# Optimization experiments

Hardware: AMD Instinct MI355X
Metric: run time of the kernel (lower is better)

Reference implementation:

```python
import jax, jax.numpy as jnp
import numpy as np

N_NODES = 100000
N_EDGES = 3200000


def gcn_conv(x, src, dst, ew, W, b, num_nodes):
    """PyG GCNConv: h = x@W; out[dst] += norm * h[src]; norm = d^-1/2[src]*w*d^-1/2[dst].
    src/dst/ew must already include self-loops (weight 1)."""
    h = x @ W  # [N, F_out]
    deg = jax.ops.segment_sum(ew, dst, num_segments=num_nodes)  # weighted in-degree
    dinv = jnp.where(deg > 0, jax.lax.rsqrt(deg), 0.0)
    norm = dinv[src] * ew * dinv[dst]  # [E]
    msg = h[src] * norm[:, None]  # [E, F_out] gather + scale
    out = jax.ops.segment_sum(msg, dst, num_segments=num_nodes)  # scatter-add
    return out + b


def setup_inputs() -> dict:
    key = jax.random.key(0)
    k1, k2, k3, k4, k5 = jax.random.split(key, 5)
    x = jax.random.normal(k1, (N_NODES, 35), dtype=jnp.float32)
    edge_index = jax.random.randint(k2, (2, N_EDGES), 0, N_NODES, dtype=jnp.int64)
    edge_weight = jax.random.uniform(k3, (N_EDGES,), dtype=jnp.float32)
    W1 = jax.random.normal(k4, (35, 64), dtype=jnp.float32) * (1.0 / np.sqrt(35))
    b1 = jnp.zeros((64,), dtype=jnp.float32)
    W2 = jax.random.normal(k5, (64, 2), dtype=jnp.float32) * (1.0 / np.sqrt(64))
    b2 = jnp.zeros((2,), dtype=jnp.float32)
    return {"x": x, "edge_index": edge_index, "edge_weight": edge_weight,
            "W1": W1, "b1": b1, "W2": W2, "b2": b2}


def reference(x, edge_index, edge_weight, W1, b1, W2, b2):
    n = x.shape[0]
    # add self-loops with weight 1 (PyG default fill_value=1), static shapes
    loop = jnp.arange(n, dtype=edge_index.dtype)
    src = jnp.concatenate([edge_index[0], loop])
    dst = jnp.concatenate([edge_index[1], loop])
    ew = jnp.concatenate([edge_weight, jnp.ones((n,), dtype=edge_weight.dtype)])

    h = jax.nn.relu(gcn_conv(x, src, dst, ew, W1, b1, n))
    h = gcn_conv(h, src, dst, ew, W2, b2, n)
    return jax.nn.log_softmax(h, axis=1)
```

## Files before the change

### kernel.cpp

```cpp
#include <hip/hip_runtime.h>
#include <hip/hip_fp16.h>
#include <math.h>

#define FIN 35
#define F1  64
#define BSZ 256
#define BSH 8
#define GSH 7
#define MAXNB 1024
#define CHUNK 16384
#define SCAP 12288

__global__ void k_hist(const int* __restrict__ dst, int* __restrict__ cmat,
                       int E, int NB, int NCHUNK) {
    __shared__ int h[MAXNB];
    int c = blockIdx.x, t = threadIdx.x;
    for (int i = t; i < NB; i += 256) h[i] = 0;
    __syncthreads();
    int e0 = c * CHUNK, e1 = min(e0 + CHUNK, E);
    bool al = ((size_t)(dst + e0) & 15) == 0;
    int nv = al ? ((e1 - e0) >> 2) : 0;
    const int4* d4 = (const int4*)(dst + e0);
    for (int i = t; i < nv; i += 256) {
        int4 v = d4[i];
        atomicAdd(&h[v.x >> BSH], 1); atomicAdd(&h[v.y >> BSH], 1);
        atomicAdd(&h[v.z >> BSH], 1); atomicAdd(&h[v.w >> BSH], 1);
    }
    for (int e = e0 + (nv << 2) + t; e < e1; e += 256) atomicAdd(&h[dst[e] >> BSH], 1);
    __syncthreads();
    for (int i = t; i < NB; i += 256) cmat[(size_t)i * NCHUNK + c] = h[i];
}

__global__ void k_scan_row(int* __restrict__ cmat, int* __restrict__ rsum, int NCHUNK) {
    __shared__ int s[256];
    int b = blockIdx.x, t = threadIdx.x;
    int v = (t < NCHUNK) ? cmat[(size_t)b * NCHUNK + t] : 0;
    s[t] = v;
    __syncthreads();
    #pragma unroll
    for (int off = 1; off < 256; off <<= 1) {
        int tv = (t >= off) ? s[t - off] : 0;
        __syncthreads();
        s[t] += tv;
        __syncthreads();
    }
    if (t < NCHUNK) cmat[(size_t)b * NCHUNK + t] = s[t] - v;
    if (t == 255) rsum[b] = s[255];
}

__global__ void k_scan_buck(const int* __restrict__ rsum, int* __restrict__ bbase,
                            int* __restrict__ boff, int NB, int E) {
    __shared__ int s[1024];
    int t = threadIdx.x;
    int v = (t < NB) ? rsum[t] : 0;
    s[t] = v;
    __syncthreads();
    #pragma unroll
    for (int off = 1; off < 1024; off <<= 1) {
        int tv = (t >= off) ? s[t - off] : 0;
        __syncthreads();
        s[t] += tv;
        __syncthreads();
    }
    if (t < NB) {
        int excl = s[t] - v;
        bbase[t] = excl;
        boff[t] = excl;
    }
    if (t == 0) boff[NB] = E;
}

__global__ void k_place(const int* __restrict__ src, const int* __restrict__ dst,
                        const float* __restrict__ ew, const int* __restrict__ cmat,
                        const int* __restrict__ bbase,
                        int2* __restrict__ recs, int E, int NB, int NCHUNK) {
    __shared__ int base[MAXNB];
    __shared__ int cur[MAXNB];
    int c = blockIdx.x, t = threadIdx.x;
    for (int i = t; i < NB; i += 256) {
        base[i] = cmat[(size_t)i * NCHUNK + c] + bbase[i];
        cur[i] = 0;
    }
    __syncthreads();
    int e0 = c * CHUNK, e1 = min(e0 + CHUNK, E);
    bool al = (((size_t)(dst + e0) | (size_t)(src + e0) | (size_t)(ew + e0)) & 15) == 0;
    int nv = al ? ((e1 - e0) >> 2) : 0;
    const int4*   s4 = (const int4*)(src + e0);
    const int4*   d4 = (const int4*)(dst + e0);
    const float4* w4 = (const float4*)(ew + e0);
    for (int i = t; i < nv; i += 256) {
        int4   sv = s4[i];
        int4   dv = d4[i];
        float4 wv = w4[i];
        int b, r;
        b = dv.x >> BSH; r = atomicAdd(&cur[b], 1);
        recs[base[b] + r] = make_int2(sv.x | ((dv.x & (BSZ-1)) << 24), __float_as_int(wv.x));
        b = dv.y >> BSH; r = atomicAdd(&cur[b], 1);
        recs[base[b] + r] = make_int2(sv.y | ((dv.y & (BSZ-1)) << 24), __float_as_int(wv.y));
        b = dv.z >> BSH; r = atomicAdd(&cur[b], 1);
        recs[base[b] + r] = make_int2(sv.z | ((dv.z & (BSZ-1)) << 24), __float_as_int(wv.z));
        b = dv.w >> BSH; r = atomicAdd(&cur[b], 1);
        recs[base[b] + r] = make_int2(sv.w | ((dv.w & (BSZ-1)) << 24), __float_as_int(wv.w));
    }
    for (int e = e0 + (nv << 2) + t; e < e1; e += 256) {
        int d = dst[e];
        int b = d >> BSH;
        int r = atomicAdd(&cur[b], 1);
        recs[base[b] + r] = make_int2(src[e] | ((d & (BSZ-1)) << 24), __float_as_int(ew[e]));
    }
}

__global__ __launch_bounds__(1024) void k_sort(
        const int* __restrict__ boff, const int2* __restrict__ recs_in,
        int2* __restrict__ recs_out, int* __restrict__ row_ptr,
        float* __restrict__ dinv, int n) {
    extern __shared__ char smem[];
    int2*   lrec  = (int2*)smem;
    unsigned short* inv16 = (unsigned short*)(lrec + SCAP);
    __shared__ int   hcnt[BSZ];
    __shared__ int   hoff[BSZ];
    __shared__ float dsum[BSZ];
    int b = blockIdx.x, t = threadIdx.x;
    if (t < BSZ) { hcnt[t] = 0; dsum[t] = 1.0f; }
    for (int i = t; i < SCAP; i += 1024) inv16[i] = 0xFFFF;
    __syncthreads();
    int s0 = boff[b], s1 = boff[b + 1];
    int cnt = s1 - s0;
    int nm = min(cnt, SCAP);
    for (int i = t; i < nm; i += 1024) {
        int2 rc = recs_in[s0 + i];
        lrec[i] = rc;
        int dl = ((unsigned)rc.x) >> 24;
        atomicAdd(&hcnt[dl], 1);
        atomicAdd(&dsum[dl], __int_as_float(rc.y));
    }
    for (int i = SCAP + t; i < cnt; i += 1024) {
        int2 rc = recs_in[s0 + i];
        int dl = ((unsigned)rc.x) >> 24;
        atomicAdd(&hcnt[dl], 1);
        atomicAdd(&dsum[dl], __int_as_float(rc.y));
    }
    __syncthreads();
    int v = 0;
    if (t < BSZ) { v = hcnt[t]; hoff[t] = v; }
    __syncthreads();
    #pragma unroll
    for (int off = 1; off < BSZ; off <<= 1) {
        int tv = 0;
        if (t < BSZ && t >= off) tv = hoff[t - off];
        __syncthreads();
        if (t < BSZ) hoff[t] += tv;
        __syncthreads();
    }
    if (t < BSZ) {
        int excl = hoff[t] - v;
        int node = b * BSZ + t;
        if (node < n) {
            row_ptr[node] = s0 + excl;
            dinv[node] = rsqrtf(dsum[t]);
            if (node == n - 1) row_ptr[n] = s1;
        }
        hcnt[t] = excl;
    }
    __syncthreads();
    for (int i = t; i < nm; i += 1024) {
        int dl = ((unsigned)lrec[i].x) >> 24;
        int pos = atomicAdd(&hcnt[dl], 1);
        if (pos < SCAP) inv16[pos] = (unsigned short)i;
        else {
            int2 rc = lrec[i];
            recs_out[s0 + pos] = make_int2((rc.x & 0xFFFFFF) << GSH, rc.y);
        }
    }
    for (int i = SCAP + t; i < cnt; i += 1024) {
        int2 rc = recs_in[s0 + i];
        int dl = ((unsigned)rc.x) >> 24;
        int pos = atomicAdd(&hcnt[dl], 1);
        recs_out[s0 + pos] = make_int2((rc.x & 0xFFFFFF) << GSH, rc.y);
    }
    __syncthreads();
    int nmo = min(cnt, SCAP);
    for (int o = t; o < nmo; o += 1024) {
        unsigned u = inv16[o];
        if (u != 0xFFFFu) {
            int2 rc = lrec[u];
            recs_out[s0 + o] = make_int2((rc.x & 0xFFFFFF) << GSH, rc.y);
        }
    }
}

__global__ void k_gemm1(const float* __restrict__ x, const float* __restrict__ W1,
                        const float* __restrict__ dinv, __half* __restrict__ g1, int n) {
    __shared__ float W1s[FIN * F1];
    __shared__ float xs[64 * FIN];
    int t = threadIdx.x;
    for (int i = t; i < FIN * F1; i += 256) W1s[i] = W1[i];
    int row0 = blockIdx.x * 64;
    int nrows = min(64, n - row0);
    for (int i = t; i < nrows * FIN; i += 256) xs[i] = x[(size_t)row0 * FIN + i];
    __syncthreads();
    int wave = t >> 6, f = t & 63;
    for (int rl = wave; rl < nrows; rl += 4) {
        float acc = 0.0f;
        #pragma unroll
        for (int k = 0; k < FIN; k++) acc += xs[rl * FIN + k] * W1s[k * F1 + f];
        int row = row0 + rl;
        g1[(size_t)row * F1 + f] = __float2half(acc * dinv[row]);
    }
}

__global__ void k_gather1(const int* __restrict__ rp, const int2* __restrict__ csr,
                          const __half* __restrict__ g1,
                          const float* __restrict__ dinv, const float* __restrict__ b1,
                          const float* __restrict__ W2, float* __restrict__ g2, int n) {
    int wid = (int)((blockIdx.x * (long long)blockDim.x + threadIdx.x) >> 6);
    int f = threadIdx.x & 63;
    if (wid >= n) return;
    const char* g1b = (const char*)g1 + f * 2;
    int start = rp[wid], end = rp[wid + 1];
    float acc = 0.0f;
    int e = start;
    for (; e + 16 <= end; e += 16) {
        float a[16];
        int2 r[16];
        #pragma unroll
        for (int j = 0; j < 16; j++) r[j] = csr[e + j];
        #pragma unroll
        for (int j = 0; j < 16; j++)
            a[j] = __half2float(*(const __half*)(g1b + (unsigned)r[j].x));
        #pragma unroll
        for (int j = 0; j < 16; j++) acc += __int_as_float(r[j].y) * a[j];
    }
    for (; e + 4 <= end; e += 4) {
        int2 r0 = csr[e], r1 = csr[e+1], r2 = csr[e+2], r3 = csr[e+3];
        float a0 = __half2float(*(const __half*)(g1b + (unsigned)r0.x));
        float a1 = __half2float(*(const __half*)(g1b + (unsigned)r1.x));
        float a2 = __half2float(*(const __half*)(g1b + (unsigned)r2.x));
        float a3 = __half2float(*(const __half*)(g1b + (unsigned)r3.x));
        acc += __int_as_float(r0.y) * a0; acc += __int_as_float(r1.y) * a1;
        acc += __int_as_float(r2.y) * a2; acc += __int_as_float(r3.y) * a3;
    }
    for (; e < end; e++) {
        int2 r = csr[e];
        acc += __int_as_float(r.y) * __half2float(*(const __half*)(g1b + (unsigned)r.x));
    }
    float dv = dinv[wid];
    float h = dv * (acc + __half2float(g1[(size_t)wid * F1 + f])) + b1[f];
    h = h > 0.0f ? h : 0.0f;
    float2 w2v = ((const float2*)W2)[f];
    float z0 = h * w2v.x, z1 = h * w2v.y;
    #pragma unroll
    for (int off = 32; off > 0; off >>= 1) {
        z0 += __shfl_xor(z0, off, 64);
        z1 += __shfl_xor(z1, off, 64);
    }
    if (f == 0) {
        g2[(size_t)wid * 2 + 0] = dv * z0;
        g2[(size_t)wid * 2 + 1] = dv * z1;
    }
}

__global__ void k_gather2(const int* __restrict__ rp, const int2* __restrict__ csr,
                          const float* __restrict__ g2,
                          const float* __restrict__ dinv, const float* __restrict__ b2,
                          float* __restrict__ out, int n) {
    int wid = (int)((blockIdx.x * (long long)blockDim.x + threadIdx.x) >> 6);
    int lane = threadIdx.x & 63;
    if (wid >= n) return;
    const char* g2b = (const char*)g2;
    int start = rp[wid], end = rp[wid + 1];
    float a0 = 0.0f, a1 = 0.0f;
    int e = start + lane;
    for (; e + 192 < end; e += 256) {
        int2 q0 = csr[e], q1 = csr[e + 64], q2 = csr[e + 128], q3 = csr[e + 192];
        float2 v0 = *(const float2*)(g2b + (((unsigned)q0.x) >> 4));
        float2 v1 = *(const float2*)(g2b + (((unsigned)q1.x) >> 4));
        float2 v2 = *(const float2*)(g2b + (((unsigned)q2.x) >> 4));
        float2 v3 = *(const float2*)(g2b + (((unsigned)q3.x) >> 4));
        a0 += __int_as_float(q0.y) * v0.x; a1 += __int_as_float(q0.y) * v0.y;
        a0 += __int_as_float(q1.y) * v1.x; a1 += __int_as_float(q1.y) * v1.y;
        a0 += __int_as_float(q2.y) * v2.x; a1 += __int_as_float(q2.y) * v2.y;
        a0 += __int_as_float(q3.y) * v3.x; a1 += __int_as_float(q3.y) * v3.y;
    }
    for (; e < end; e += 64) {
        int2 r = csr[e];
        float w = __int_as_float(r.y);
        float2 gv = *(const float2*)(g2b + (((unsigned)r.x) >> 4));
        a0 += w * gv.x; a1 += w * gv.y;
    }
    #pragma unroll
    for (int off = 32; off > 0; off >>= 1) {
        a0 += __shfl_xor(a0, off, 64);
        a1 += __shfl_xor(a1, off, 64);
    }
    if (lane == 0) {
        float dv = dinv[wid];
        float2 sv = ((const float2*)g2)[wid];
        float z0 = dv * (a0 + sv.x) + b2[0];
        float z1 = dv * (a1 + sv.y) + b2[1];
        float m = fmaxf(z0, z1);
        float lse = m + logf(expf(z0 - m) + expf(z1 - m));
        ((float2*)out)[wid] = make_float2(z0 - lse, z1 - lse);
    }
}

extern "C" void kernel_launch(void* const* d_in, const int* in_sizes, int n_in,
                              void* d_out, int out_size, void* d_ws, size_t ws_size,
                              hipStream_t stream) {
    const float* x  = (const float*)d_in[0];
    const int*   ei = (const int*)d_in[1];
    const float* ew = (const float*)d_in[2];
    const float* W1 = (const float*)d_in[3];
    const float* b1 = (const float*)d_in[4];
    const float* W2 = (const float*)d_in[5];
    const float* b2 = (const float*)d_in[6];
    float* out = (float*)d_out;

    int n = in_sizes[0] / FIN;
    int E = in_sizes[2];
    const int* src = ei;
    const int* dst = ei + E;
    int NB = (n + BSZ - 1) / BSZ;
    int NCHUNK = (E + CHUNK - 1) / CHUNK;
    int M = NB * NCHUNK;

    char* ws = (char*)d_ws;
    size_t off = 0;
    auto alloc = [&](size_t bytes) -> void* {
        void* p = ws + off;
        off += (bytes + 15) & ~(size_t)15;
        return p;
    };
    int*    cmat    = (int*)   alloc((size_t)M * 4);
    int*    rsum    = (int*)   alloc((size_t)NB * 4);
    int*    bbase   = (int*)   alloc((size_t)NB * 4);
    int*    boff    = (int*)   alloc((size_t)(NB + 1) * 4);
    int*    row_ptr = (int*)   alloc((size_t)(n + 1) * 4);
    float*  dinv    = (float*) alloc((size_t)n * 4);
    int2*   recs_a  = (int2*)  alloc((size_t)E * 8);
    int2*   recs_b  = (int2*)  alloc((size_t)E * 8);
    __half* g1      = (__half*)alloc((size_t)n * F1 * 2);
    float*  g2      = (float*) alloc((size_t)n * 2 * 4);

    size_t sort_lds = (size_t)SCAP * 8 + (size_t)SCAP * 2;

    k_hist     <<<NCHUNK, 256, 0, stream>>>(dst, cmat, E, NB, NCHUNK);
    k_scan_row <<<NB, 256, 0, stream>>>(cmat, rsum, NCHUNK);
    k_scan_buck<<<1, 1024, 0, stream>>>(rsum, bbase, boff, NB, E);
    k_place    <<<NCHUNK, 256, 0, stream>>>(src, dst, ew, cmat, bbase, recs_a, E, NB, NCHUNK);
    k_sort     <<<NB, 1024, sort_lds, stream>>>(boff, recs_a, recs_b, row_ptr, dinv, n);
    k_gemm1    <<<(n + 63) / 64, 256, 0, stream>>>(x, W1, dinv, g1, n);
    k_gather1  <<<(n + 3) / 4, 256, 0, stream>>>(row_ptr, recs_b, g1, dinv, b1, W2, g2, n);
    k_gather2  <<<(n + 3) / 4, 256, 0, stream>>>(row_ptr, recs_b, g2, dinv, b2, out, n);
}
```

Baseline: 319.8 us.

## Stage bucketed records in LDS before global scatter; shrink sort LDS footprint

k_place now builds a local per-chunk histogram and prefix scan, writes records into LDS grouped by bucket together with their global destination addresses, then writes them out in local order so consecutive threads hit contiguous global runs. Chunks are halved and blocks use 512 threads, which doubles the number of chunks and the width of the scan kernels. k_sort no longer caches records in LDS; it re-reads them from global memory through a 16-bit permutation index, cutting its LDS use so more blocks can be resident. The trade is extra global reads in k_sort, plus NB is now limited to 512 buckets and NCHUNK to 512.

```diff
diff --git a/kernel.cpp b/kernel.cpp
--- a/kernel.cpp
+++ b/kernel.cpp
@@ -7,8 +7,8 @@
 #define BSZ 256
 #define BSH 8
 #define GSH 7
-#define MAXNB 1024
-#define CHUNK 16384
+#define MAXNB 512
+#define PCH 8192
 #define SCAP 12288
 
 __global__ void k_hist(const int* __restrict__ dst, int* __restrict__ cmat,
@@ -17,7 +17,7 @@
     int c = blockIdx.x, t = threadIdx.x;
     for (int i = t; i < NB; i += 256) h[i] = 0;
     __syncthreads();
-    int e0 = c * CHUNK, e1 = min(e0 + CHUNK, E);
+    int e0 = c * PCH, e1 = min(e0 + PCH, E);
     bool al = ((size_t)(dst + e0) & 15) == 0;
     int nv = al ? ((e1 - e0) >> 2) : 0;
     const int4* d4 = (const int4*)(dst + e0);
@@ -32,20 +32,20 @@
 }
 
 __global__ void k_scan_row(int* __restrict__ cmat, int* __restrict__ rsum, int NCHUNK) {
-    __shared__ int s[256];
+    __shared__ int s[512];
     int b = blockIdx.x, t = threadIdx.x;
     int v = (t < NCHUNK) ? cmat[(size_t)b * NCHUNK + t] : 0;
     s[t] = v;
     __syncthreads();
     #pragma unroll
-    for (int off = 1; off < 256; off <<= 1) {
+    for (int off = 1; off < 512; off <<= 1) {
         int tv = (t >= off) ? s[t - off] : 0;
         __syncthreads();
         s[t] += tv;
         __syncthreads();
     }
     if (t < NCHUNK) cmat[(size_t)b * NCHUNK + t] = s[t] - v;
-    if (t == 255) rsum[b] = s[255];
+    if (t == 511) rsum[b] = s[511];
 }
 
 __global__ void k_scan_buck(const int* __restrict__ rsum, int* __restrict__ bbase,
@@ -70,71 +70,92 @@
     if (t == 0) boff[NB] = E;
 }
 
-__global__ void k_place(const int* __restrict__ src, const int* __restrict__ dst,
-                        const float* __restrict__ ew, const int* __restrict__ cmat,
-                        const int* __restrict__ bbase,
-                        int2* __restrict__ recs, int E, int NB, int NCHUNK) {
-    __shared__ int base[MAXNB];
-    __shared__ int cur[MAXNB];
+__global__ __launch_bounds__(512) void k_place(
+        const int* __restrict__ src, const int* __restrict__ dst,
+        const float* __restrict__ ew, const int* __restrict__ cmat,
+        const int* __restrict__ bbase,
+        int2* __restrict__ recs, int E, int NB, int NCHUNK) {
+    extern __shared__ char pmem[];
+    int2* lrec   = (int2*)pmem;
+    int*  addr32 = (int*)(lrec + PCH);
+    __shared__ int s[512];
+    __shared__ int lbase[512];
+    __shared__ int cur[512];
+    __shared__ int gwin[512];
     int c = blockIdx.x, t = threadIdx.x;
-    for (int i = t; i < NB; i += 256) {
-        base[i] = cmat[(size_t)i * NCHUNK + c] + bbase[i];
-        cur[i] = 0;
-    }
-    __syncthreads();
-    int e0 = c * CHUNK, e1 = min(e0 + CHUNK, E);
+    s[t] = 0;
+    __syncthreads();
+    int e0 = c * PCH, e1 = min(e0 + PCH, E);
     bool al = (((size_t)(dst + e0) | (size_t)(src + e0) | (size_t)(ew + e0)) & 15) == 0;
     int nv = al ? ((e1 - e0) >> 2) : 0;
     const int4*   s4 = (const int4*)(src + e0);
     const int4*   d4 = (const int4*)(dst + e0);
     const float4* w4 = (const float4*)(ew + e0);
-    for (int i = t; i < nv; i += 256) {
+    for (int i = t; i < nv; i += 512) {
+        int4 v = d4[i];
+        atomicAdd(&s[v.x >> BSH], 1); atomicAdd(&s[v.y >> BSH], 1);
+        atomicAdd(&s[v.z >> BSH], 1); atomicAdd(&s[v.w >> BSH], 1);
+    }
+    for (int e = e0 + (nv << 2) + t; e < e1; e += 512) atomicAdd(&s[dst[e] >> BSH], 1);
+    __syncthreads();
+    int v = s[t];
+    __syncthreads();
+    #pragma unroll
+    for (int off = 1; off < 512; off <<= 1) {
+        int tv = (t >= off) ? s[t - off] : 0;
+        __syncthreads();
+        s[t] += tv;
+        __syncthreads();
+    }
+    lbase[t] = s[t] - v;
+    cur[t] = 0;
+    gwin[t] = (t < NB) ? (cmat[(size_t)t * NCHUNK + c] + bbase[t]) : 0;
+    __syncthreads();
+    for (int i = t; i < nv; i += 512) {
         int4   sv = s4[i];
         int4   dv = d4[i];
         float4 wv = w4[i];
-        int b, r;
-        b = dv.x >> BSH; r = atomicAdd(&cur[b], 1);
-        recs[base[b] + r] = make_int2(sv.x | ((dv.x & (BSZ-1)) << 24), __float_as_int(wv.x));
-        b = dv.y >> BSH; r = atomicAdd(&cur[b], 1);
-        recs[base[b] + r] = make_int2(sv.y | ((dv.y & (BSZ-1)) << 24), __float_as_int(wv.y));
-        b = dv.z >> BSH; r = atomicAdd(&cur[b], 1);
-        recs[base[b] + r] = make_int2(sv.z | ((dv.z & (BSZ-1)) << 24), __float_as_int(wv.z));
-        b = dv.w >> BSH; r = atomicAdd(&cur[b], 1);
-        recs[base[b] + r] = make_int2(sv.w | ((dv.w & (BSZ-1)) << 24), __float_as_int(wv.w));
-    }
-    for (int e = e0 + (nv << 2) + t; e < e1; e += 256) {
+        int b, r, sl;
+        b = dv.x >> BSH; r = atomicAdd(&cur[b], 1); sl = lbase[b] + r;
+        lrec[sl] = make_int2(sv.x | ((dv.x & (BSZ-1)) << 24), __float_as_int(wv.x));
+        addr32[sl] = gwin[b] + r;
+        b = dv.y >> BSH; r = atomicAdd(&cur[b], 1); sl = lbase[b] + r;
+        lrec[sl] = make_int2(sv.y | ((dv.y & (BSZ-1)) << 24), __float_as_int(wv.y));
+        addr32[sl] = gwin[b] + r;
+        b = dv.z >> BSH; r = atomicAdd(&cur[b], 1); sl = lbase[b] + r;
+        lrec[sl] = make_int2(sv.z | ((dv.z & (BSZ-1)) << 24), __float_as_int(wv.z));
+        addr32[sl] = gwin[b] + r;
+        b = dv.w >> BSH; r = atomicAdd(&cur[b], 1); sl = lbase[b] + r;
+        lrec[sl] = make_int2(sv.w | ((dv.w & (BSZ-1)) << 24), __float_as_int(wv.w));
+        addr32[sl] = gwin[b] + r;
+    }
+    for (int e = e0 + (nv << 2) + t; e < e1; e += 512) {
         int d = dst[e];
         int b = d >> BSH;
         int r = atomicAdd(&cur[b], 1);
-        recs[base[b] + r] = make_int2(src[e] | ((d & (BSZ-1)) << 24), __float_as_int(ew[e]));
-    }
+        int sl = lbase[b] + r;
+        lrec[sl] = make_int2(src[e] | ((d & (BSZ-1)) << 24), __float_as_int(ew[e]));
+        addr32[sl] = gwin[b] + r;
+    }
+    __syncthreads();
+    int cnt = e1 - e0;
+    for (int i = t; i < cnt; i += 512) recs[addr32[i]] = lrec[i];
 }
 
 __global__ __launch_bounds__(1024) void k_sort(
         const int* __restrict__ boff, const int2* __restrict__ recs_in,
         int2* __restrict__ recs_out, int* __restrict__ row_ptr,
         float* __restrict__ dinv, int n) {
-    extern __shared__ char smem[];
-    int2*   lrec  = (int2*)smem;
-    unsigned short* inv16 = (unsigned short*)(lrec + SCAP);
+    extern __shared__ unsigned short inv16[];
     __shared__ int   hcnt[BSZ];
     __shared__ int   hoff[BSZ];
     __shared__ float dsum[BSZ];
     int b = blockIdx.x, t = threadIdx.x;
     if (t < BSZ) { hcnt[t] = 0; dsum[t] = 1.0f; }
-    for (int i = t; i < SCAP; i += 1024) inv16[i] = 0xFFFF;
     __syncthreads();
     int s0 = boff[b], s1 = boff[b + 1];
     int cnt = s1 - s0;
-    int nm = min(cnt, SCAP);
-    for (int i = t; i < nm; i += 1024) {
-        int2 rc = recs_in[s0 + i];
-        lrec[i] = rc;
-        int dl = ((unsigned)rc.x) >> 24;
-        atomicAdd(&hcnt[dl], 1);
-        atomicAdd(&dsum[dl], __int_as_float(rc.y));
-    }
-    for (int i = SCAP + t; i < cnt; i += 1024) {
+    for (int i = t; i < cnt; i += 1024) {
         int2 rc = recs_in[s0 + i];
         int dl = ((unsigned)rc.x) >> 24;
         atomicAdd(&hcnt[dl], 1);
@@ -163,28 +184,24 @@
         hcnt[t] = excl;
     }
     __syncthreads();
-    for (int i = t; i < nm; i += 1024) {
-        int dl = ((unsigned)lrec[i].x) >> 24;
-        int pos = atomicAdd(&hcnt[dl], 1);
-        if (pos < SCAP) inv16[pos] = (unsigned short)i;
-        else {
-            int2 rc = lrec[i];
+    if (cnt <= SCAP) {
+        for (int i = t; i < cnt; i += 1024) {
+            int2 rc = recs_in[s0 + i];
+            int dl = ((unsigned)rc.x) >> 24;
+            int pos = atomicAdd(&hcnt[dl], 1);
+            inv16[pos] = (unsigned short)i;
+        }
+        __syncthreads();
+        for (int o = t; o < cnt; o += 1024) {
+            int2 rc = recs_in[s0 + inv16[o]];
+            recs_out[s0 + o] = make_int2((rc.x & 0xFFFFFF) << GSH, rc.y);
+        }
+    } else {
+        for (int i = t; i < cnt; i += 1024) {
+            int2 rc = recs_in[s0 + i];
+            int dl = ((unsigned)rc.x) >> 24;
+            int pos = atomicAdd(&hcnt[dl], 1);
             recs_out[s0 + pos] = make_int2((rc.x & 0xFFFFFF) << GSH, rc.y);
-        }
-    }
-    for (int i = SCAP + t; i < cnt; i += 1024) {
-        int2 rc = recs_in[s0 + i];
-        int dl = ((unsigned)rc.x) >> 24;
-        int pos = atomicAdd(&hcnt[dl], 1);
-        recs_out[s0 + pos] = make_int2((rc.x & 0xFFFFFF) << GSH, rc.y);
-    }
-    __syncthreads();
-    int nmo = min(cnt, SCAP);
-    for (int o = t; o < nmo; o += 1024) {
-        unsigned u = inv16[o];
-        if (u != 0xFFFFu) {
-            int2 rc = lrec[u];
-            recs_out[s0 + o] = make_int2((rc.x & 0xFFFFFF) << GSH, rc.y);
         }
     }
 }
@@ -321,7 +338,7 @@
     const int* src = ei;
     const int* dst = ei + E;
     int NB = (n + BSZ - 1) / BSZ;
-    int NCHUNK = (E + CHUNK - 1) / CHUNK;
+    int NCHUNK = (E + PCH - 1) / PCH;
     int M = NB * NCHUNK;
 
     char* ws = (char*)d_ws;
@@ -342,12 +359,13 @@
     __half* g1      = (__half*)alloc((size_t)n * F1 * 2);
     float*  g2      = (float*) alloc((size_t)n * 2 * 4);
 
-    size_t sort_lds = (size_t)SCAP * 8 + (size_t)SCAP * 2;
+    size_t place_lds = (size_t)PCH * 8 + (size_t)PCH * 4;
+    size_t sort_lds  = (size_t)SCAP * 2;
 
     k_hist     <<<NCHUNK, 256, 0, stream>>>(dst, cmat, E, NB, NCHUNK);
-    k_scan_row <<<NB, 256, 0, stream>>>(cmat, rsum, NCHUNK);
+    k_scan_row <<<NB, 512, 0, stream>>>(cmat, rsum, NCHUNK);
     k_scan_buck<<<1, 1024, 0, stream>>>(rsum, bbase, boff, NB, E);
-    k_place    <<<NCHUNK, 256, 0, stream>>>(src, dst, ew, cmat, bbase, recs_a, E, NB, NCHUNK);
+    k_place    <<<NCHUNK, 512, place_lds, stream>>>(src, dst, ew, cmat, bbase, recs_a, E, NB, NCHUNK);
     k_sort     <<<NB, 1024, sort_lds, stream>>>(boff, recs_a, recs_b, row_ptr, dinv, n);
     k_gemm1    <<<(n + 63) / 64, 256, 0, stream>>>(x, W1, dinv, g1, n);
     k_gather1  <<<(n + 3) / 4, 256, 0, stream>>>(row_ptr, recs_b, g1, dinv, b1, W2, g2, n);
```

After: 305.7 us. 1.05x faster.
